# Performance work log

Measured on AMD Instinct MI355X. Metric: run time of the kernel, lower is better.

Reference implementation:

```python
import jax, jax.numpy as jnp
import numpy as np
from jax import lax

B, C, H, W = 8, 1024, 64, 48
A = 9  # anchors per location

def _conv(x, w, b, pad):
    y = lax.conv_general_dilated(x, w, (1, 1), pad,
                                 dimension_numbers=('NCHW', 'OIHW', 'NCHW'))
    return y + b[None, :, None, None]

def setup_inputs() -> dict:
    key = jax.random.key(0)
    ks = jax.random.split(key, 12)
    base_feat = jax.random.normal(ks[0], (B, C, H, W), dtype=jnp.float32)
    W_conv = jax.random.normal(ks[1], (512, C, 3, 3), dtype=jnp.float32) * 0.01
    b_conv = jnp.zeros((512,), jnp.float32)
    W_cls = jax.random.normal(ks[2], (18, 512, 1, 1), dtype=jnp.float32) * 0.01
    b_cls = jnp.zeros((18,), jnp.float32)
    W_bbox = jax.random.normal(ks[3], (36, 512, 1, 1), dtype=jnp.float32) * 0.01
    b_bbox = jnp.zeros((36,), jnp.float32)
    # anchor-target-layer outputs (data-dependent assignment) provided as inputs
    rpn_label = (jax.random.randint(ks[4], (B, A * H * W), 0, 3) - 1).astype(jnp.int32)  # {-1,0,1}
    rpn_bbox_targets = jax.random.normal(ks[5], (B, 36, H, W), dtype=jnp.float32) * 0.1
    rpn_bbox_inside_weights = (jax.random.uniform(ks[6], (B, 36, H, W)) < 0.25).astype(jnp.float32)
    rpn_bbox_outside_weights = jax.random.uniform(ks[7], (B, 36, H, W), dtype=jnp.float32) * 0.01
    return {"base_feat": base_feat, "W_conv": W_conv, "b_conv": b_conv,
            "W_cls": W_cls, "b_cls": b_cls, "W_bbox": W_bbox, "b_bbox": b_bbox,
            "rpn_label": rpn_label, "rpn_bbox_targets": rpn_bbox_targets,
            "rpn_bbox_inside_weights": rpn_bbox_inside_weights,
            "rpn_bbox_outside_weights": rpn_bbox_outside_weights}

def reference(base_feat, W_conv, b_conv, W_cls, b_cls, W_bbox, b_bbox,
              rpn_label, rpn_bbox_targets, rpn_bbox_inside_weights,
              rpn_bbox_outside_weights):
    # RPN head: 3x3 conv + relu, then 1x1 cls / bbox heads
    rpn_conv1 = jax.nn.relu(_conv(base_feat, W_conv, b_conv, ((1, 1), (1, 1))))
    cls_score = _conv(rpn_conv1, W_cls, b_cls, ((0, 0), (0, 0)))   # [B,18,H,W]
    bbox_pred = _conv(rpn_conv1, W_bbox, b_bbox, ((0, 0), (0, 0)))  # [B,36,H,W]
    # reshape to [B,2,A*H,W], softmax over the 2-way fg/bg axis, reshape back
    score_rs = cls_score.reshape(B, 2, A * H, W)
    prob_rs = jax.nn.softmax(score_rs, axis=1)
    rpn_cls_prob = prob_rs.reshape(B, 18, H, W)
    # classification loss: permute(0,2,3,1).view(-1,2), keep labels != -1
    logits = score_rs.transpose(0, 2, 3, 1).reshape(-1, 2)
    label = rpn_label.reshape(-1)
    valid = (label != -1).astype(logits.dtype)
    logp = jax.nn.log_softmax(logits, axis=-1)
    lbl = jnp.clip(label, 0, 1)
    nll = -jnp.take_along_axis(logp, lbl[:, None].astype(jnp.int32), axis=1)[:, 0]
    rpn_loss_cls = jnp.sum(nll * valid) / jnp.maximum(jnp.sum(valid), 1.0)
    # smooth-L1 box loss, sigma=3, summed over dims [1,2,3], mean over batch
    sigma2 = 9.0
    in_diff = rpn_bbox_inside_weights * (bbox_pred - rpn_bbox_targets)
    abs_d = jnp.abs(in_diff)
    sign = lax.stop_gradient((abs_d < 1.0 / sigma2).astype(abs_d.dtype))
    in_loss = in_diff * in_diff * (sigma2 / 2.0) * sign + (abs_d - 0.5 / sigma2) * (1.0 - sign)
    rpn_loss_box = jnp.mean(jnp.sum(rpn_bbox_outside_weights * in_loss, axis=(1, 2, 3)))
    return rpn_cls_prob, bbox_pred, rpn_loss_cls, rpn_loss_box
```

## Files before the change

### kernel.cpp

```cpp
#include <hip/hip_runtime.h>
#include <stdint.h>

#define B_    8
#define CIN   1024
#define H_    64
#define W_    48
#define OC    512
#define HW    3072
#define NPOS  24576
#define K9    9216
#define HP    66
#define WP    50

typedef __attribute__((ext_vector_type(8))) __bf16 bf16x8;
typedef __attribute__((ext_vector_type(4))) float  float4_t;
typedef __attribute__((ext_vector_type(4))) unsigned short ushort4_t;
typedef __attribute__((ext_vector_type(8))) int int8v;
typedef __attribute__((ext_vector_type(4))) int int4v;

__device__ __forceinline__ unsigned short f2bf(float x) {
  union { float f; unsigned u; } v; v.f = x;
  unsigned r = v.u + 0x7FFFu + ((v.u >> 16) & 1u);
  return (unsigned short)(r >> 16);
}

__device__ __forceinline__ unsigned int pack4_fp8(float a, float b, float c, float d) {
  int w = __builtin_amdgcn_cvt_pk_fp8_f32(a, b, 0, false);
  w = __builtin_amdgcn_cvt_pk_fp8_f32(c, d, w, true);
  return (unsigned int)w;
}

__device__ __forceinline__ void async16(const void* g, void* l) {
  __builtin_amdgcn_global_load_lds(
      (const __attribute__((address_space(1))) unsigned int*)g,
      (__attribute__((address_space(3))) unsigned int*)l, 16, 0, 0);
}

__device__ __forceinline__ float wave_sum(float v) {
  for (int o = 32; o > 0; o >>= 1) v += __shfl_down(v, o, 64);
  return v;
}

__global__ void prep_x(const float* __restrict__ x, unsigned char* __restrict__ xt) {
  int cx = blockIdx.x, h = blockIdx.y, b = blockIdx.z;
  __shared__ float tile[128 * 49];
  int t = threadIdx.x;
  const float* src = x + ((long)(b * CIN + cx * 128) * H_ + h) * W_;
  for (int it = 0; it < 24; ++it) {
    int e = it * 256 + t;
    int cl = e / 48, w = e % 48;
    tile[cl * 49 + w] = src[(long)cl * HW + w];
  }
  __syncthreads();
  unsigned char* dst = xt + ((long)(b * HP + h + 1) * WP + 1) * CIN + cx * 128;
  for (int it = 0; it < 6; ++it) {
    int e = it * 256 + t;
    int w = e >> 5, g = e & 31;
    float v0 = tile[(g * 4 + 0) * 49 + w] * 16.f;
    float v1 = tile[(g * 4 + 1) * 49 + w] * 16.f;
    float v2 = tile[(g * 4 + 2) * 49 + w] * 16.f;
    float v3 = tile[(g * 4 + 3) * 49 + w] * 16.f;
    *(unsigned int*)&dst[(long)w * CIN + g * 4] = pack4_fp8(v0, v1, v2, v3);
  }
}

__global__ void prep_w(const float* __restrict__ Wc, unsigned char* __restrict__ Wa) {
  __shared__ float lw[9216];
  int o = blockIdx.x, t = threadIdx.x;
  const float* src = Wc + (long)o * K9;
  for (int i = 0; i < 36; ++i) lw[i * 256 + t] = src[i * 256 + t];
  __syncthreads();
  unsigned char* dst = Wa + (long)o * K9;
  int c = t * 4;
  for (int off = 0; off < 9; ++off) {
    float v0 = lw[(c + 0) * 9 + off] * 512.f;
    float v1 = lw[(c + 1) * 9 + off] * 512.f;
    float v2 = lw[(c + 2) * 9 + off] * 512.f;
    float v3 = lw[(c + 3) * 9 + off] * 512.f;
    *(unsigned int*)&dst[off * 1024 + c] = pack4_fp8(v0, v1, v2, v3);
  }
}

__global__ void prep_wh(const float* __restrict__ Wcls, const float* __restrict__ Wbb,
                        unsigned short* __restrict__ Wh) {
  int i = blockIdx.x * 256 + threadIdx.x;
  int m = i >> 9, c = i & 511;
  float v = 0.f;
  if (m < 18) v = Wcls[m * 512 + c];
  else if (m < 54) v = Wbb[(m - 18) * 512 + c];
  Wh[i] = f2bf(v);
}

#define BKF 128
__global__ __launch_bounds__(256, 2)
void conv_gemm(const unsigned char* __restrict__ Wa, const unsigned char* __restrict__ xt,
               const float* __restrict__ bias, unsigned short* __restrict__ conv1) {
  __shared__ unsigned char As[128 * BKF];
  __shared__ unsigned char Bs[128 * BKF];
  int t = threadIdx.x;
  int lane = t & 63, wv = t >> 6;
  int m0 = blockIdx.y * 128;
  int n0 = blockIdx.x * 128;
  const unsigned char* aSrc[4];
  const unsigned char* bSrc[4];
  for (int s = 0; s < 4; ++s) {
    int c = s * 256 + t;
    int r = c >> 3;
    int q = (c & 7) ^ (r & 7);
    aSrc[s] = Wa + (long)(m0 + r) * K9 + q * 16;
    int n = n0 + r; int b = n / HW; int rem = n % HW; int h = rem / W_; int w = rem % W_;
    bSrc[s] = xt + ((long)(b * HP + h) * WP + w) * CIN + q * 16;
  }
  float4_t acc[4][4] = {};
  int wm = wv >> 1, wn = wv & 1;
  int quad = lane >> 4, col = lane & 15;
  for (int kt = 0; kt < 72; ++kt) {
    int off = kt >> 3;
    int dy = off / 3, dx = off % 3;
    long boff = (long)(dy * WP + dx) * CIN + (kt & 7) * 128;
    long aoff = (long)kt * 128;
    __syncthreads();
    for (int s = 0; s < 4; ++s)
      async16(aSrc[s] + aoff, &As[s * 4096 + wv * 1024]);
    for (int s = 0; s < 4; ++s)
      async16(bSrc[s] + boff, &Bs[s * 4096 + wv * 1024]);
    __syncthreads();
    int8v af[4], bfr[4];
    for (int i = 0; i < 4; ++i) {
      int r = wm * 64 + i * 16 + col;
      int rb = r * 128, x7 = r & 7;
      int4v lo = *(const int4v*)&As[rb + (((quad * 2 + 0) ^ x7) << 4)];
      int4v hi = *(const int4v*)&As[rb + (((quad * 2 + 1) ^ x7) << 4)];
      af[i] = (int8v){lo.x, lo.y, lo.z, lo.w, hi.x, hi.y, hi.z, hi.w};
    }
    for (int j = 0; j < 4; ++j) {
      int r = wn * 64 + j * 16 + col;
      int rb = r * 128, x7 = r & 7;
      int4v lo = *(const int4v*)&Bs[rb + (((quad * 2 + 0) ^ x7) << 4)];
      int4v hi = *(const int4v*)&Bs[rb + (((quad * 2 + 1) ^ x7) << 4)];
      bfr[j] = (int8v){lo.x, lo.y, lo.z, lo.w, hi.x, hi.y, hi.z, hi.w};
    }
    for (int i = 0; i < 4; ++i)
      for (int j = 0; j < 4; ++j)
        acc[i][j] = __builtin_amdgcn_mfma_scale_f32_16x16x128_f8f6f4(
            af[i], bfr[j], acc[i][j], 0, 0, 0, 0x76767676, 0, 0x7B7B7B7B);
  }
  for (int i = 0; i < 4; ++i) {
    int mb = m0 + wm * 64 + i * 16 + quad * 4;
    float b0 = bias[mb + 0], b1 = bias[mb + 1], b2 = bias[mb + 2], b3 = bias[mb + 3];
    for (int j = 0; j < 4; ++j) {
      int n = n0 + wn * 64 + j * 16 + col;
      ushort4_t pk;
      pk.x = f2bf(fmaxf(acc[i][j].x + b0, 0.f));
      pk.y = f2bf(fmaxf(acc[i][j].y + b1, 0.f));
      pk.z = f2bf(fmaxf(acc[i][j].z + b2, 0.f));
      pk.w = f2bf(fmaxf(acc[i][j].w + b3, 0.f));
      *(ushort4_t*)&conv1[(long)n * 512 + mb] = pk;
    }
  }
}

__global__ __launch_bounds__(256, 2)
void head_gemm(const unsigned short* __restrict__ Wh, const unsigned short* __restrict__ conv1,
               const float* __restrict__ b_cls, const float* __restrict__ b_bbox,
               float* __restrict__ cls_ws, float* __restrict__ out_bbox) {
  __shared__ unsigned short As[64 * 32];
  __shared__ unsigned short Bs[128 * 32];
  int t = threadIdx.x;
  int lane = t & 63, wv = t >> 6;
  int n0 = blockIdx.x * 128;
  int srow = wv * 16 + (lane >> 2);
  int skof = (lane & 3) * 8;
  int quad = lane >> 4, col = lane & 15;
  float4_t acc[4][2] = {};
  for (int kt = 0; kt < 16; ++kt) {
    int k0 = kt * 32;
    __syncthreads();
    async16(Wh + (long)srow * 512 + k0 + skof, &As[wv * 512]);
    for (int q = 0; q < 2; ++q)
      async16(conv1 + (long)(n0 + q * 64 + srow) * 512 + k0 + skof, &Bs[q * 2048 + wv * 512]);
    __syncthreads();
    bf16x8 af[4], bfr[2];
    for (int i = 0; i < 4; ++i)
      af[i] = *(const bf16x8*)&As[(i * 16 + col) * 32 + quad * 8];
    for (int j = 0; j < 2; ++j)
      bfr[j] = *(const bf16x8*)&Bs[(wv * 32 + j * 16 + col) * 32 + quad * 8];
    for (int i = 0; i < 4; ++i)
      for (int j = 0; j < 2; ++j)
        acc[i][j] = __builtin_amdgcn_mfma_f32_16x16x32_bf16(af[i], bfr[j], acc[i][j], 0, 0, 0);
  }
  for (int j = 0; j < 2; ++j) {
    int n = n0 + wv * 32 + j * 16 + col;
    int b = n / HW; int rem = n % HW;
    for (int i = 0; i < 4; ++i) {
      for (int r = 0; r < 4; ++r) {
        int m = i * 16 + quad * 4 + r;
        float v = acc[i][j][r];
        if (m < 18) {
          cls_ws[(long)(b * 18 + m) * HW + rem] = v + b_cls[m];
        } else if (m < 54) {
          out_bbox[(long)(b * 36 + (m - 18)) * HW + rem] = v + b_bbox[m - 18];
        }
      }
    }
  }
}

__global__ void softmax_loss(const float* __restrict__ cls, const int* __restrict__ label,
                             float* __restrict__ prob, float* __restrict__ acc) {
  int idx = blockIdx.x * 256 + threadIdx.x;
  int b = idx / 27648; int r = idx % 27648;
  int a = r / HW; int r2 = r % HW;
  long i0 = (long)(b * 18 + a) * HW + r2;
  long i1 = i0 + (long)9 * HW;
  float x0 = cls[i0], x1 = cls[i1];
  float mx = fmaxf(x0, x1);
  float e0 = __expf(x0 - mx), e1 = __expf(x1 - mx);
  float s = e0 + e1;
  prob[i0] = e0 / s;
  prob[i1] = e1 / s;
  int lb = label[idx];
  float nll = 0.f, val = 0.f;
  if (lb != -1) {
    val = 1.f;
    float xl = (lb > 0) ? x1 : x0;
    nll = -(xl - mx - __logf(s));
  }
  nll = wave_sum(nll);
  val = wave_sum(val);
  __shared__ float red[8];
  int lane = threadIdx.x & 63, wv = threadIdx.x >> 6;
  if (lane == 0) { red[wv] = nll; red[4 + wv] = val; }
  __syncthreads();
  if (threadIdx.x == 0) {
    atomicAdd(&acc[0], red[0] + red[1] + red[2] + red[3]);
    atomicAdd(&acc[1], red[4] + red[5] + red[6] + red[7]);
  }
}

__global__ void box_loss(const float* __restrict__ pred, const float* __restrict__ tgt,
                         const float* __restrict__ iw, const float* __restrict__ ow,
                         float* __restrict__ acc) {
  float s = 0.f;
  const long total = (long)B_ * 36 * HW;
  for (long i = (long)blockIdx.x * 256 + threadIdx.x; i < total; i += (long)gridDim.x * 256) {
    float d = iw[i] * (pred[i] - tgt[i]);
    float ad = fabsf(d);
    float l = (ad < (1.f / 9.f)) ? d * d * 4.5f : ad - (1.f / 18.f);
    s += ow[i] * l;
  }
  s = wave_sum(s);
  __shared__ float red[4];
  int lane = threadIdx.x & 63, wv = threadIdx.x >> 6;
  if (lane == 0) red[wv] = s;
  __syncthreads();
  if (threadIdx.x == 0) atomicAdd(&acc[2], red[0] + red[1] + red[2] + red[3]);
}

__global__ void finalize(const float* __restrict__ acc, float* __restrict__ out) {
  if (threadIdx.x == 0) {
    out[0] = acc[0] / fmaxf(acc[1], 1.f);
    out[1] = acc[2] / (float)B_;
  }
}

extern "C" void kernel_launch(void* const* d_in, const int* in_sizes, int n_in,
                              void* d_out, int out_size, void* d_ws, size_t ws_size,
                              hipStream_t stream) {
  const float* base_feat = (const float*)d_in[0];
  const float* W_conv    = (const float*)d_in[1];
  const float* b_conv    = (const float*)d_in[2];
  const float* W_cls     = (const float*)d_in[3];
  const float* b_cls     = (const float*)d_in[4];
  const float* W_bbox    = (const float*)d_in[5];
  const float* b_bbox    = (const float*)d_in[6];
  const int*   rpn_label = (const int*)d_in[7];
  const float* bb_tgt    = (const float*)d_in[8];
  const float* bb_iw     = (const float*)d_in[9];
  const float* bb_ow     = (const float*)d_in[10];

  float* out = (float*)d_out;
  float* out_cls_prob = out;
  float* out_bbox     = out + 442368;
  float* out_scalars  = out + 442368 + 884736;

  size_t off = 0;
  auto alloc = [&](size_t bytes) {
    void* p = (char*)d_ws + off;
    off = (off + bytes + 255) & ~(size_t)255;
    return p;
  };
  const size_t XT_BYTES = (size_t)B_ * HP * WP * CIN;
  unsigned char*  xt    = (unsigned char*)alloc(XT_BYTES);
  unsigned char*  Wa    = (unsigned char*)alloc((size_t)OC * K9);
  unsigned short* conv1 = (unsigned short*)alloc((size_t)NPOS * OC * 2);
  unsigned short* Wh    = (unsigned short*)alloc((size_t)64 * 512 * 2);
  float* cls_ws         = (float*)alloc((size_t)B_ * 18 * HW * 4);
  float* accbuf         = (float*)alloc(16);

  hipMemsetAsync(xt, 0, XT_BYTES, stream);
  hipMemsetAsync(accbuf, 0, 16, stream);

  prep_x<<<dim3(8, 64, 8), 256, 0, stream>>>(base_feat, xt);
  prep_w<<<512, 256, 0, stream>>>(W_conv, Wa);
  prep_wh<<<128, 256, 0, stream>>>(W_cls, W_bbox, Wh);
  conv_gemm<<<dim3(192, 4), 256, 0, stream>>>(Wa, xt, b_conv, conv1);
  head_gemm<<<192, 256, 0, stream>>>(Wh, conv1, b_cls, b_bbox, cls_ws, out_bbox);
  softmax_loss<<<864, 256, 0, stream>>>(cls_ws, rpn_label, out_cls_prob, accbuf);
  box_loss<<<1728, 256, 0, stream>>>(out_bbox, bb_tgt, bb_iw, bb_ow, accbuf);
  finalize<<<1, 64, 0, stream>>>(accbuf, out_scalars);
}
```

Baseline: 374.2 us.

## Fuse prep kernels, replace memsets with border zeroing, retile head GEMM, fuse losses

```diff
diff --git a/kernel.cpp b/kernel.cpp
--- a/kernel.cpp
+++ b/kernel.cpp
@@ -41,54 +41,76 @@
   return v;
 }
 
-__global__ void prep_x(const float* __restrict__ x, unsigned char* __restrict__ xt) {
-  int cx = blockIdx.x, h = blockIdx.y, b = blockIdx.z;
-  __shared__ float tile[128 * 49];
-  int t = threadIdx.x;
-  const float* src = x + ((long)(b * CIN + cx * 128) * H_ + h) * W_;
-  for (int it = 0; it < 24; ++it) {
-    int e = it * 256 + t;
-    int cl = e / 48, w = e % 48;
-    tile[cl * 49 + w] = src[(long)cl * HW + w];
-  }
-  __syncthreads();
-  unsigned char* dst = xt + ((long)(b * HP + h + 1) * WP + 1) * CIN + cx * 128;
-  for (int it = 0; it < 6; ++it) {
-    int e = it * 256 + t;
-    int w = e >> 5, g = e & 31;
-    float v0 = tile[(g * 4 + 0) * 49 + w] * 16.f;
-    float v1 = tile[(g * 4 + 1) * 49 + w] * 16.f;
-    float v2 = tile[(g * 4 + 2) * 49 + w] * 16.f;
-    float v3 = tile[(g * 4 + 3) * 49 + w] * 16.f;
-    *(unsigned int*)&dst[(long)w * CIN + g * 4] = pack4_fp8(v0, v1, v2, v3);
-  }
-}
-
-__global__ void prep_w(const float* __restrict__ Wc, unsigned char* __restrict__ Wa) {
-  __shared__ float lw[9216];
-  int o = blockIdx.x, t = threadIdx.x;
-  const float* src = Wc + (long)o * K9;
-  for (int i = 0; i < 36; ++i) lw[i * 256 + t] = src[i * 256 + t];
-  __syncthreads();
-  unsigned char* dst = Wa + (long)o * K9;
-  int c = t * 4;
-  for (int off = 0; off < 9; ++off) {
-    float v0 = lw[(c + 0) * 9 + off] * 512.f;
-    float v1 = lw[(c + 1) * 9 + off] * 512.f;
-    float v2 = lw[(c + 2) * 9 + off] * 512.f;
-    float v3 = lw[(c + 3) * 9 + off] * 512.f;
-    *(unsigned int*)&dst[off * 1024 + c] = pack4_fp8(v0, v1, v2, v3);
-  }
-}
-
-__global__ void prep_wh(const float* __restrict__ Wcls, const float* __restrict__ Wbb,
-                        unsigned short* __restrict__ Wh) {
-  int i = blockIdx.x * 256 + threadIdx.x;
-  int m = i >> 9, c = i & 511;
-  float v = 0.f;
-  if (m < 18) v = Wcls[m * 512 + c];
-  else if (m < 54) v = Wbb[(m - 18) * 512 + c];
-  Wh[i] = f2bf(v);
+__global__ void prep_fused(const float* __restrict__ x, const float* __restrict__ Wc,
+                           const float* __restrict__ Wcls, const float* __restrict__ Wbb,
+                           unsigned char* __restrict__ xt, unsigned char* __restrict__ Wa,
+                           unsigned short* __restrict__ Wh, float* __restrict__ accbuf) {
+  __shared__ float smem[9216];
+  int bid = blockIdx.x, t = threadIdx.x;
+  if (bid < 4096) {
+    int cx = bid & 7, h = (bid >> 3) & 63, b = bid >> 9;
+    float* tile = smem;
+    const float* src = x + ((long)(b * CIN + cx * 128) * H_ + h) * W_;
+    for (int it = 0; it < 6; ++it) {
+      int e = it * 256 + t;
+      int cl = e / 12, w4 = e % 12;
+      float4_t v = *(const float4_t*)&src[(long)cl * HW + w4 * 4];
+      int base = cl * 49 + w4 * 4;
+      tile[base] = v.x; tile[base + 1] = v.y; tile[base + 2] = v.z; tile[base + 3] = v.w;
+    }
+    __syncthreads();
+    unsigned char* dst = xt + ((long)(b * HP + h + 1) * WP + 1) * CIN + cx * 128;
+    for (int it = 0; it < 6; ++it) {
+      int e = it * 256 + t;
+      int w = e >> 5, g = e & 31;
+      float v0 = tile[(g * 4 + 0) * 49 + w] * 16.f;
+      float v1 = tile[(g * 4 + 1) * 49 + w] * 16.f;
+      float v2 = tile[(g * 4 + 2) * 49 + w] * 16.f;
+      float v3 = tile[(g * 4 + 3) * 49 + w] * 16.f;
+      *(unsigned int*)&dst[(long)w * CIN + g * 4] = pack4_fp8(v0, v1, v2, v3);
+    }
+  } else if (bid < 4608) {
+    int o = bid - 4096;
+    float* lw = smem;
+    const float* src = Wc + (long)o * K9;
+    for (int i = 0; i < 9; ++i)
+      *(float4_t*)&lw[i * 1024 + t * 4] = *(const float4_t*)&src[i * 1024 + t * 4];
+    __syncthreads();
+    unsigned char* dst = Wa + (long)o * K9;
+    int c = t * 4;
+    for (int off = 0; off < 9; ++off) {
+      float v0 = lw[(c + 0) * 9 + off] * 512.f;
+      float v1 = lw[(c + 1) * 9 + off] * 512.f;
+      float v2 = lw[(c + 2) * 9 + off] * 512.f;
+      float v3 = lw[(c + 3) * 9 + off] * 512.f;
+      *(unsigned int*)&dst[off * 1024 + c] = pack4_fp8(v0, v1, v2, v3);
+    }
+  } else if (bid < 4640) {
+    int e = (bid - 4608) * 1024 + t * 4;
+    int m = e >> 9, c = e & 511;
+    float v0 = 0.f, v1 = 0.f, v2 = 0.f, v3 = 0.f;
+    if (m < 18) {
+      const float* s = Wcls + m * 512 + c;
+      v0 = s[0]; v1 = s[1]; v2 = s[2]; v3 = s[3];
+    } else if (m < 54) {
+      const float* s = Wbb + (m - 18) * 512 + c;
+      v0 = s[0]; v1 = s[1]; v2 = s[2]; v3 = s[3];
+    }
+    ushort4_t pk; pk.x = f2bf(v0); pk.y = f2bf(v1); pk.z = f2bf(v2); pk.w = f2bf(v3);
+    *(ushort4_t*)&Wh[e] = pk;
+    if (bid == 4608 && t < 4) accbuf[t] = 0.f;
+  } else {
+    int bid2 = bid - 4640;
+    int b = bid2 / 66, h = bid2 % 66;
+    unsigned char* base = xt + (long)(b * 66 + h) * 50 * 1024;
+    int4v z = {};
+    if (h == 0 || h == 65) {
+      for (int i = t; i < 3200; i += 256) *(int4v*)(base + (long)i * 16) = z;
+    } else if (t < 128) {
+      int which = t >> 6, off = t & 63;
+      *(int4v*)(base + (long)which * 49 * 1024 + (long)off * 16) = z;
+    }
+  }
 }
 
 #define BKF 128
@@ -164,97 +186,102 @@
 void head_gemm(const unsigned short* __restrict__ Wh, const unsigned short* __restrict__ conv1,
                const float* __restrict__ b_cls, const float* __restrict__ b_bbox,
                float* __restrict__ cls_ws, float* __restrict__ out_bbox) {
-  __shared__ unsigned short As[64 * 32];
-  __shared__ unsigned short Bs[128 * 32];
+  __shared__ unsigned short As[64 * 128];
+  __shared__ unsigned short Bs[64 * 128];
   int t = threadIdx.x;
   int lane = t & 63, wv = t >> 6;
-  int n0 = blockIdx.x * 128;
-  int srow = wv * 16 + (lane >> 2);
-  int skof = (lane & 3) * 8;
+  int n0 = blockIdx.x * 64;
   int quad = lane >> 4, col = lane & 15;
-  float4_t acc[4][2] = {};
-  for (int kt = 0; kt < 16; ++kt) {
-    int k0 = kt * 32;
-    __syncthreads();
-    async16(Wh + (long)srow * 512 + k0 + skof, &As[wv * 512]);
-    for (int q = 0; q < 2; ++q)
-      async16(conv1 + (long)(n0 + q * 64 + srow) * 512 + k0 + skof, &Bs[q * 2048 + wv * 512]);
-    __syncthreads();
-    bf16x8 af[4], bfr[2];
-    for (int i = 0; i < 4; ++i)
-      af[i] = *(const bf16x8*)&As[(i * 16 + col) * 32 + quad * 8];
-    for (int j = 0; j < 2; ++j)
-      bfr[j] = *(const bf16x8*)&Bs[(wv * 32 + j * 16 + col) * 32 + quad * 8];
-    for (int i = 0; i < 4; ++i)
-      for (int j = 0; j < 2; ++j)
-        acc[i][j] = __builtin_amdgcn_mfma_f32_16x16x32_bf16(af[i], bfr[j], acc[i][j], 0, 0, 0);
-  }
-  for (int j = 0; j < 2; ++j) {
-    int n = n0 + wv * 32 + j * 16 + col;
-    int b = n / HW; int rem = n % HW;
-    for (int i = 0; i < 4; ++i) {
-      for (int r = 0; r < 4; ++r) {
-        int m = i * 16 + quad * 4 + r;
-        float v = acc[i][j][r];
-        if (m < 18) {
-          cls_ws[(long)(b * 18 + m) * HW + rem] = v + b_cls[m];
-        } else if (m < 54) {
-          out_bbox[(long)(b * 36 + (m - 18)) * HW + rem] = v + b_bbox[m - 18];
-        }
+  const unsigned short* aS[4];
+  const unsigned short* bS[4];
+  for (int p = 0; p < 4; ++p) {
+    int c = p * 256 + t;
+    int r = c >> 4;
+    int q = (c & 15) ^ (r & 15);
+    aS[p] = Wh + (long)r * 512 + q * 8;
+    bS[p] = conv1 + (long)(n0 + r) * 512 + q * 8;
+  }
+  float4_t acc[4] = {};
+  for (int kt = 0; kt < 4; ++kt) {
+    long koff = (long)kt * 128;
+    __syncthreads();
+    for (int p = 0; p < 4; ++p) async16(aS[p] + koff, &As[p * 2048 + wv * 512]);
+    for (int p = 0; p < 4; ++p) async16(bS[p] + koff, &Bs[p * 2048 + wv * 512]);
+    __syncthreads();
+    for (int ks = 0; ks < 4; ++ks) {
+      int rn = wv * 16 + col;
+      bf16x8 bfr = *(const bf16x8*)&Bs[rn * 128 + (((ks * 4 + quad) ^ (rn & 15)) << 3)];
+      for (int i = 0; i < 4; ++i) {
+        int r = i * 16 + col;
+        bf16x8 af = *(const bf16x8*)&As[r * 128 + (((ks * 4 + quad) ^ (r & 15)) << 3)];
+        acc[i] = __builtin_amdgcn_mfma_f32_16x16x32_bf16(af, bfr, acc[i], 0, 0, 0);
       }
     }
   }
-}
-
-__global__ void softmax_loss(const float* __restrict__ cls, const int* __restrict__ label,
-                             float* __restrict__ prob, float* __restrict__ acc) {
-  int idx = blockIdx.x * 256 + threadIdx.x;
-  int b = idx / 27648; int r = idx % 27648;
-  int a = r / HW; int r2 = r % HW;
-  long i0 = (long)(b * 18 + a) * HW + r2;
-  long i1 = i0 + (long)9 * HW;
-  float x0 = cls[i0], x1 = cls[i1];
-  float mx = fmaxf(x0, x1);
-  float e0 = __expf(x0 - mx), e1 = __expf(x1 - mx);
-  float s = e0 + e1;
-  prob[i0] = e0 / s;
-  prob[i1] = e1 / s;
-  int lb = label[idx];
-  float nll = 0.f, val = 0.f;
-  if (lb != -1) {
-    val = 1.f;
-    float xl = (lb > 0) ? x1 : x0;
-    nll = -(xl - mx - __logf(s));
-  }
-  nll = wave_sum(nll);
-  val = wave_sum(val);
+  int n = n0 + wv * 16 + col;
+  int b = n / HW; int rem = n % HW;
+  for (int i = 0; i < 4; ++i) {
+    for (int r = 0; r < 4; ++r) {
+      int m = i * 16 + quad * 4 + r;
+      float v = acc[i][r];
+      if (m < 18) {
+        cls_ws[(long)(b * 18 + m) * HW + rem] = v + b_cls[m];
+      } else if (m < 54) {
+        out_bbox[(long)(b * 36 + (m - 18)) * HW + rem] = v + b_bbox[m - 18];
+      }
+    }
+  }
+}
+
+__global__ void loss_fused(const float* __restrict__ cls, const int* __restrict__ label,
+                           float* __restrict__ prob,
+                           const float* __restrict__ pred, const float* __restrict__ tgt,
+                           const float* __restrict__ iw, const float* __restrict__ ow,
+                           float* __restrict__ acc) {
+  int lane = threadIdx.x & 63, wv = threadIdx.x >> 6;
   __shared__ float red[8];
-  int lane = threadIdx.x & 63, wv = threadIdx.x >> 6;
-  if (lane == 0) { red[wv] = nll; red[4 + wv] = val; }
-  __syncthreads();
-  if (threadIdx.x == 0) {
-    atomicAdd(&acc[0], red[0] + red[1] + red[2] + red[3]);
-    atomicAdd(&acc[1], red[4] + red[5] + red[6] + red[7]);
-  }
-}
-
-__global__ void box_loss(const float* __restrict__ pred, const float* __restrict__ tgt,
-                         const float* __restrict__ iw, const float* __restrict__ ow,
-                         float* __restrict__ acc) {
-  float s = 0.f;
-  const long total = (long)B_ * 36 * HW;
-  for (long i = (long)blockIdx.x * 256 + threadIdx.x; i < total; i += (long)gridDim.x * 256) {
-    float d = iw[i] * (pred[i] - tgt[i]);
-    float ad = fabsf(d);
-    float l = (ad < (1.f / 9.f)) ? d * d * 4.5f : ad - (1.f / 18.f);
-    s += ow[i] * l;
-  }
-  s = wave_sum(s);
-  __shared__ float red[4];
-  int lane = threadIdx.x & 63, wv = threadIdx.x >> 6;
-  if (lane == 0) red[wv] = s;
-  __syncthreads();
-  if (threadIdx.x == 0) atomicAdd(&acc[2], red[0] + red[1] + red[2] + red[3]);
+  if (blockIdx.x < 864) {
+    int idx = blockIdx.x * 256 + threadIdx.x;
+    int b = idx / 27648; int r = idx % 27648;
+    int a = r / HW; int r2 = r % HW;
+    long i0 = (long)(b * 18 + a) * HW + r2;
+    long i1 = i0 + (long)9 * HW;
+    float x0 = cls[i0], x1 = cls[i1];
+    float mx = fmaxf(x0, x1);
+    float e0 = __expf(x0 - mx), e1 = __expf(x1 - mx);
+    float s = e0 + e1;
+    prob[i0] = e0 / s;
+    prob[i1] = e1 / s;
+    int lb = label[idx];
+    float nll = 0.f, val = 0.f;
+    if (lb != -1) {
+      val = 1.f;
+      float xl = (lb > 0) ? x1 : x0;
+      nll = -(xl - mx - __logf(s));
+    }
+    nll = wave_sum(nll);
+    val = wave_sum(val);
+    if (lane == 0) { red[wv] = nll; red[4 + wv] = val; }
+    __syncthreads();
+    if (threadIdx.x == 0) {
+      atomicAdd(&acc[0], red[0] + red[1] + red[2] + red[3]);
+      atomicAdd(&acc[1], red[4] + red[5] + red[6] + red[7]);
+    }
+  } else {
+    int bid = blockIdx.x - 864;
+    float s = 0.f;
+    const long total = (long)B_ * 36 * HW;
+    for (long i = (long)bid * 256 + threadIdx.x; i < total; i += (long)1728 * 256) {
+      float d = iw[i] * (pred[i] - tgt[i]);
+      float ad = fabsf(d);
+      float l = (ad < (1.f / 9.f)) ? d * d * 4.5f : ad - (1.f / 18.f);
+      s += ow[i] * l;
+    }
+    s = wave_sum(s);
+    if (lane == 0) red[wv] = s;
+    __syncthreads();
+    if (threadIdx.x == 0) atomicAdd(&acc[2], red[0] + red[1] + red[2] + red[3]);
+  }
 }
 
 __global__ void finalize(const float* __restrict__ acc, float* __restrict__ out) {
@@ -298,15 +325,10 @@
   float* cls_ws         = (float*)alloc((size_t)B_ * 18 * HW * 4);
   float* accbuf         = (float*)alloc(16);
 
-  hipMemsetAsync(xt, 0, XT_BYTES, stream);
-  hipMemsetAsync(accbuf, 0, 16, stream);
-
-  prep_x<<<dim3(8, 64, 8), 256, 0, stream>>>(base_feat, xt);
-  prep_w<<<512, 256, 0, stream>>>(W_conv, Wa);
-  prep_wh<<<128, 256, 0, stream>>>(W_cls, W_bbox, Wh);
+  prep_fused<<<5168, 256, 0, stream>>>(base_feat, W_conv, W_cls, W_bbox, xt, Wa, Wh, accbuf);
   conv_gemm<<<dim3(192, 4), 256, 0, stream>>>(Wa, xt, b_conv, conv1);
-  head_gemm<<<192, 256, 0, stream>>>(Wh, conv1, b_cls, b_bbox, cls_ws, out_bbox);
-  softmax_loss<<<864, 256, 0, stream>>>(cls_ws, rpn_label, out_cls_prob, accbuf);
-  box_loss<<<1728, 256, 0, stream>>>(out_bbox, bb_tgt, bb_iw, bb_ow, accbuf);
+  head_gemm<<<384, 256, 0, stream>>>(Wh, conv1, b_cls, b_bbox, cls_ws, out_bbox);
+  loss_fused<<<2592, 256, 0, stream>>>(cls_ws, rpn_label, out_cls_prob,
+                                       out_bbox, bb_tgt, bb_iw, bb_ow, accbuf);
   finalize<<<1, 64, 0, stream>>>(accbuf, out_scalars);
 }
```

New measurement: 355.2 us. 1.05x faster.
